# Kernel tuning notes

Hardware: AMD Instinct MI355X
Metric: run time of the kernel (lower is better)

Reference implementation:

```python
import math
import jax, jax.numpy as jnp
import numpy as np

B, C = 4, 128
H_B, W_B = 512, 512          # BEV size
H_C, W_C = 64, 2048          # cylinder size (z-bins x phi)
MAX_RANGE = 50.0
XMIN, XMAX, YMIN, YMAX = -50.0, 50.0, -50.0, 50.0


def setup_inputs() -> dict:
    key = jax.random.key(0)
    bev_feat = jax.random.normal(key, (B, C, H_B, W_B), dtype=jnp.float32)
    return {"bev_feat": bev_feat}


def reference(bev_feat):
    # Build sampling locations. In the torch module the pixel coords are
    # normalized to [-1,1] and grid_sample(align_corners=True) un-normalizes
    # them back to exactly x_pix / y_pix, so we sample at pixel coords directly.
    phi = jnp.linspace(-math.pi, math.pi, W_C)
    x_g = MAX_RANGE * jnp.cos(phi)
    y_g = MAX_RANGE * jnp.sin(phi)
    x = (x_g - XMIN) / (XMAX - XMIN) * (W_B - 1)   # [W_C] pixel x
    y = (YMAX - y_g) / (YMAX - YMIN) * (H_B - 1)   # [W_C] pixel y

    # Bilinear interpolation with zero padding. The grid is identical for
    # every cylinder row, so sample once per phi column and broadcast.
    x0 = jnp.floor(x).astype(jnp.int32); x1 = x0 + 1
    y0 = jnp.floor(y).astype(jnp.int32); y1 = y0 + 1
    wx1 = x - x0; wx0 = 1.0 - wx1
    wy1 = y - y0; wy0 = 1.0 - wy1

    def corner(xi, yi, w):
        valid = (xi >= 0) & (xi < W_B) & (yi >= 0) & (yi < H_B)
        xi_c = jnp.clip(xi, 0, W_B - 1)
        yi_c = jnp.clip(yi, 0, H_B - 1)
        v = bev_feat[:, :, yi_c, xi_c]            # [B, C, W_C]
        return v * (w * valid)[None, None, :]

    col = (corner(x0, y0, wx0 * wy0) + corner(x1, y0, wx1 * wy0)
           + corner(x0, y1, wx0 * wy1) + corner(x1, y1, wx1 * wy1))
    # broadcast across the H_C z-bins -> [B, C, H_C, W_C]
    return jnp.broadcast_to(col[:, :, None, :], (col.shape[0], col.shape[1], H_C, W_C))
```

## Files before the change

kernel.cpp:

```cpp
#include <hip/hip_runtime.h>
#include <math.h>


namespace {
constexpr int BB = 4, CC = 128, HB = 512, WB = 512, HC = 64, WC = 2048;
constexpr float XMIN = -50.0f, XMAX = 50.0f, YMIN = -50.0f, YMAX = 50.0f;
constexpr float MAX_RANGE = 50.0f;

__device__ __forceinline__ float sample_col(const float* __restrict__ img, int j) {
    const float PI = 3.14159265358979323846f;
    float phi = -PI + (float)j * (2.0f * PI / (float)(WC - 1));
    float xg = MAX_RANGE * cosf(phi);
    float yg = MAX_RANGE * sinf(phi);
    float x = (xg - XMIN) * ((float)(WB - 1) / (XMAX - XMIN));
    float y = (YMAX - yg) * ((float)(HB - 1) / (YMAX - YMIN));
    float fx0 = floorf(x), fy0 = floorf(y);
    int x0 = (int)fx0, y0 = (int)fy0;
    int x1 = x0 + 1, y1 = y0 + 1;
    float wx1 = x - fx0, wx0 = 1.0f - wx1;
    float wy1 = y - fy0, wy0 = 1.0f - wy1;

    float acc = 0.0f;
    {
        bool v = (x0 >= 0) & (x0 < WB) & (y0 >= 0) & (y0 < HB);
        int xc = min(max(x0, 0), WB - 1), yc = min(max(y0, 0), HB - 1);
        acc += img[yc * WB + xc] * (v ? wx0 * wy0 : 0.0f);
    }
    {
        bool v = (x1 >= 0) & (x1 < WB) & (y0 >= 0) & (y0 < HB);
        int xc = min(max(x1, 0), WB - 1), yc = min(max(y0, 0), HB - 1);
        acc += img[yc * WB + xc] * (v ? wx1 * wy0 : 0.0f);
    }
    {
        bool v = (x0 >= 0) & (x0 < WB) & (y1 >= 0) & (y1 < HB);
        int xc = min(max(x0, 0), WB - 1), yc = min(max(y1, 0), HB - 1);
        acc += img[yc * WB + xc] * (v ? wx0 * wy1 : 0.0f);
    }
    {
        bool v = (x1 >= 0) & (x1 < WB) & (y1 >= 0) & (y1 < HB);
        int xc = min(max(x1, 0), WB - 1), yc = min(max(y1, 0), HB - 1);
        acc += img[yc * WB + xc] * (v ? wx1 * wy1 : 0.0f);
    }
    return acc;
}
}

__global__ __launch_bounds__(256) void bev2cyl_kernel(const float* __restrict__ bev,
                                                      float* __restrict__ out) {
    int t = blockIdx.x * 256 + threadIdx.x;
    int bc = t >> 9;
    int jq = t & 511;
    int j0 = jq << 2;

    const float* img = bev + (size_t)bc * (size_t)(HB * WB);

    float4 v;
    v.x = sample_col(img, j0 + 0);
    v.y = sample_col(img, j0 + 1);
    v.z = sample_col(img, j0 + 2);
    v.w = sample_col(img, j0 + 3);

    float* o = out + (size_t)bc * (size_t)(HC * WC) + j0;
#pragma unroll 8
    for (int h = 0; h < HC; ++h) {
        *(float4*)o = v;
        o += WC;
    }
}

extern "C" void kernel_launch(void* const* d_in, const int* in_sizes, int n_in,
                              void* d_out, int out_size, void* d_ws, size_t ws_size,
                              hipStream_t stream) {
    const float* bev = (const float*)d_in[0];
    float* out = (float*)d_out;
    dim3 grid(BB * CC * WC / 4 / 256);
    dim3 block(256);
    bev2cyl_kernel<<<grid, block, 0, stream>>>(bev, out);
}
```

Before: 668.7 us.

## Split into column-sampling kernel and flat broadcast-store kernel via workspace

The single fused kernel, where each thread sampled four columns and then wrote 64 strided float4 rows, is replaced by two kernels. The first computes the sampled column into the workspace with one thread per column. The second does a fully parallel, contiguous float4 write of the output, re-reading the small column buffer, which should stay in cache. The aim is to spread the 268 MB of output stores across many more threads and waves. The cost is an extra launch and a round trip through the workspace buffer.

Result: no change. 664.8 us (-0.6%).

```diff
diff --git a/kernel.cpp b/kernel.cpp
--- a/kernel.cpp
+++ b/kernel.cpp
@@ -45,27 +45,24 @@
 }
 }
 
-__global__ __launch_bounds__(256) void bev2cyl_kernel(const float* __restrict__ bev,
-                                                      float* __restrict__ out) {
+__global__ __launch_bounds__(256) void col_kernel(const float* __restrict__ bev,
+                                                  float* __restrict__ col) {
     int t = blockIdx.x * 256 + threadIdx.x;
-    int bc = t >> 9;
-    int jq = t & 511;
-    int j0 = jq << 2;
+    int bc = t >> 11;
+    int j  = t & (WC - 1);
+    const float* img = bev + (size_t)bc * (size_t)(HB * WB);
+    col[t] = sample_col(img, j);
+}
 
-    const float* img = bev + (size_t)bc * (size_t)(HB * WB);
-
-    float4 v;
-    v.x = sample_col(img, j0 + 0);
-    v.y = sample_col(img, j0 + 1);
-    v.z = sample_col(img, j0 + 2);
-    v.w = sample_col(img, j0 + 3);
-
-    float* o = out + (size_t)bc * (size_t)(HC * WC) + j0;
-#pragma unroll 8
-    for (int h = 0; h < HC; ++h) {
-        *(float4*)o = v;
-        o += WC;
-    }
+__global__ __launch_bounds__(256) void bcast_kernel(const float* __restrict__ col,
+                                                    float* __restrict__ out) {
+    int t = blockIdx.x * 256 + threadIdx.x;
+    int bc = t >> 15;
+    int r  = t & 32767;
+    int jq = r & 511;
+    const float4* colv = (const float4*)col;
+    float4 v = colv[(bc << 9) + jq];
+    ((float4*)out)[t] = v;
 }
 
 extern "C" void kernel_launch(void* const* d_in, const int* in_sizes, int n_in,
@@ -73,7 +70,8 @@
                               hipStream_t stream) {
     const float* bev = (const float*)d_in[0];
     float* out = (float*)d_out;
-    dim3 grid(BB * CC * WC / 4 / 256);
-    dim3 block(256);
-    bev2cyl_kernel<<<grid, block, 0, stream>>>(bev, out);
+    float* col = (float*)d_ws;
+
+    col_kernel<<<dim3(BB * CC * WC / 256), dim3(256), 0, stream>>>(bev, col);
+    bcast_kernel<<<dim3(BB * CC * HC * WC / 4 / 256), dim3(256), 0, stream>>>(col, out);
 }
```
